# Performance work log

Measured on AMD Instinct MI355X. Metric: run time of the kernel, lower is better.

The kernel has to match this reference:

```python
import jax, jax.numpy as jnp
import numpy as np

B, L, V, H, N, NL = 32, 1024, 32000, 512, 64, 4


def setup_inputs() -> dict:
    key = jax.random.key(0)
    ks = jax.random.split(key, 10)
    x = jax.random.randint(ks[0], (B, L), 0, V)
    embedding = jax.random.normal(ks[1], (V, H), jnp.float32) * 0.02
    # S4D-style init: dt log-uniform in [1e-3, 1e-1], A = -0.5 + i*pi*n (S4D-Lin)
    log_dt = jax.random.uniform(ks[2], (NL, H), jnp.float32,
                                minval=np.log(1e-3), maxval=np.log(1e-1))
    A_log = jnp.log(0.5 * jnp.ones((NL, H, N), jnp.float32))
    A_imag = jnp.broadcast_to(np.pi * jnp.arange(N, dtype=jnp.float32), (NL, H, N))
    C_re = jax.random.normal(ks[3], (NL, H, N), jnp.float32) * (0.5 ** 0.5)
    C_im = jax.random.normal(ks[4], (NL, H, N), jnp.float32) * (0.5 ** 0.5)
    D = jax.random.normal(ks[5], (NL, H), jnp.float32)
    fc_w = jax.random.normal(ks[6], (1, H), jnp.float32) * (1.0 / np.sqrt(H))
    fc_b = jnp.zeros((1,), jnp.float32)
    return {"x": x, "embedding": embedding, "log_dt": log_dt, "A_log": A_log,
            "A_imag": A_imag, "C_re": C_re, "C_im": C_im, "D": D,
            "fc_w": fc_w, "fc_b": fc_b}


def _s4d_layer(u, log_dt, A_log, A_imag, C_re, C_im, D):
    # u: [B, L, H] -> channels-first [B, H, L]
    Lx = u.shape[1]
    ub = jnp.transpose(u, (0, 2, 1))
    dt = jnp.exp(log_dt)                              # [H]
    A = -jnp.exp(A_log) + 1j * A_imag                 # [H, N]
    dtA = dt[:, None] * A                             # [H, N]
    C = C_re + 1j * C_im
    Ct = C * (jnp.exp(dtA) - 1.0) / A                 # ZOH-discretized C*B
    t = jnp.arange(Lx, dtype=jnp.float32)
    vand = jnp.exp(dtA[:, :, None] * t)               # [H, N, L] Vandermonde
    K = 2.0 * jnp.einsum('hn,hnl->hl', Ct, vand).real # [H, L] SSM kernel
    n = 2 * Lx                                        # linear conv via padded FFT
    y = jnp.fft.irfft(jnp.fft.rfft(ub, n=n) * jnp.fft.rfft(K, n=n), n=n)[..., :Lx]
    y = y + D[:, None] * ub                           # skip connection
    y = jax.nn.gelu(y)
    return jnp.transpose(y, (0, 2, 1))                # [B, L, H]


def reference(x, embedding, log_dt, A_log, A_imag, C_re, C_im, D, fc_w, fc_b):
    h = embedding[x]                                  # [B, L, H]
    for i in range(log_dt.shape[0]):                  # small fixed layer count
        h = _s4d_layer(h, log_dt[i], A_log[i], A_imag[i],
                       C_re[i], C_im[i], D[i])
    pooled = h.mean(axis=1)                           # [B, H]
    out = pooled @ fc_w.T + fc_b                      # [B, 1]
    return out.squeeze(1)                             # [B]
```

## Files before the change

### kernel.cpp

```cpp
#include <hip/hip_runtime.h>
#include <math.h>

static const int kB = 32;
static const int kL = 1024;
static const int kH = 512;
static const int kN = 64;
static const int kNL = 4;
static const int kNFFT = 2048;

#define TWO_PI 6.283185307179586476925286766559

typedef float v2f __attribute__((ext_vector_type(2)));

__device__ __forceinline__ v2f cmul(v2f a, v2f b) {
    v2f axx = __builtin_shufflevector(a, a, 0, 0);
    v2f ayy = __builtin_shufflevector(a, a, 1, 1);
    v2f byx = __builtin_shufflevector(b, b, 1, 0);
    v2f t = ayy * byx;
    t.x = -t.x;
    return axx * b + t;
}

template<bool INV>
__device__ __forceinline__ v2f jrot(v2f t) {
    v2f r = __builtin_shufflevector(t, t, 1, 0);
    if (!INV) { r.y = -r.y; } else { r.x = -r.x; }
    return r;
}

#define LDSZ 2176
__device__ __forceinline__ constexpr int swoff(int LGM, int u) {
    return (LGM == 0) ? u : (LGM == 3) ? (8 * u + (u >> 1)) : (68 * u);
}

template<bool INV>
__device__ __forceinline__ void dft8(const v2f c[8], v2f y[8]) {
    const float s = 0.70710678118654752440f;
    v2f t0 = c[0] + c[4], t1 = c[0] - c[4];
    v2f t2 = c[2] + c[6], t3 = c[2] - c[6];
    v2f e0 = t0 + t2, e2 = t0 - t2;
    v2f j3 = jrot<INV>(t3);
    v2f e1 = t1 + j3, e3 = t1 - j3;

    t0 = c[1] + c[5]; t1 = c[1] - c[5];
    t2 = c[3] + c[7]; t3 = c[3] - c[7];
    v2f o0 = t0 + t2, o2 = t0 - t2;
    v2f j3o = jrot<INV>(t3);
    v2f o1 = t1 + j3o, o3 = t1 - j3o;

    if (!INV) {
        v2f r1 = __builtin_shufflevector(o1, o1, 1, 0);
        o1 = s * (v2f){o1.x + r1.x, o1.y - r1.y};
        v2f r2 = __builtin_shufflevector(o2, o2, 1, 0);
        o2 = (v2f){r2.x, -r2.y};
        v2f r3 = __builtin_shufflevector(o3, o3, 1, 0);
        o3 = s * (v2f){r3.x - o3.x, -r3.y - o3.y};
    } else {
        v2f r1 = __builtin_shufflevector(o1, o1, 1, 0);
        o1 = s * (v2f){o1.x - r1.x, o1.y + r1.y};
        v2f r2 = __builtin_shufflevector(o2, o2, 1, 0);
        o2 = (v2f){-r2.x, r2.y};
        v2f r3 = __builtin_shufflevector(o3, o3, 1, 0);
        o3 = s * (v2f){-(o3.x + r3.x), r3.y - o3.y};
    }
    y[0] = e0 + o0; y[4] = e0 - o0;
    y[1] = e1 + o1; y[5] = e1 - o1;
    y[2] = e2 + o2; y[6] = e2 - o2;
    y[3] = e3 + o3; y[7] = e3 - o3;
}

__device__ __forceinline__ void dft8h(const v2f c[4], v2f y[8]) {
    const float s = 0.70710678118654752440f;
    v2f e0 = c[0] + c[2], e2 = c[0] - c[2];
    v2f j  = jrot<false>(c[2]);
    v2f e1 = c[0] + j, e3 = c[0] - j;
    v2f o0 = c[1] + c[3], o2 = c[1] - c[3];
    v2f jo = jrot<false>(c[3]);
    v2f o1 = c[1] + jo, o3 = c[1] - jo;

    v2f r1 = __builtin_shufflevector(o1, o1, 1, 0);
    o1 = s * (v2f){o1.x + r1.x, o1.y - r1.y};
    v2f r2 = __builtin_shufflevector(o2, o2, 1, 0);
    o2 = (v2f){r2.x, -r2.y};
    v2f r3 = __builtin_shufflevector(o3, o3, 1, 0);
    o3 = s * (v2f){r3.x - o3.x, -r3.y - o3.y};

    y[0] = e0 + o0; y[4] = e0 - o0;
    y[1] = e1 + o1; y[5] = e1 - o1;
    y[2] = e2 + o2; y[6] = e2 - o2;
    y[3] = e3 + o3; y[7] = e3 - o3;
}

template<bool INV, int LGM>
__device__ __forceinline__ void stage8_write(v2f* lds, int tid, v2f y[8]) {
    const int m = 1 << LGM;
    const int jm = tid & ~(m - 1);
    float rev = (INV ? (1.0f / 2048.0f) : (-1.0f / 2048.0f)) * (float)jm;
    v2f w1 = { __builtin_amdgcn_cosf(rev), __builtin_amdgcn_sinf(rev) };
    v2f w2 = cmul(w1, w1);
    v2f w3 = cmul(w2, w1);
    v2f w4 = cmul(w2, w2);
    v2f w5 = cmul(w3, w2);
    v2f w6 = cmul(w3, w3);
    v2f w7 = cmul(w4, w3);
    int base = ((tid >> LGM) << (LGM + 3)) + (tid & (m - 1));
    int swb = base + (base >> 4);
    lds[swb + swoff(LGM, 0)] = y[0];
    lds[swb + swoff(LGM, 1)] = cmul(w1, y[1]);
    lds[swb + swoff(LGM, 2)] = cmul(w2, y[2]);
    lds[swb + swoff(LGM, 3)] = cmul(w3, y[3]);
    lds[swb + swoff(LGM, 4)] = cmul(w4, y[4]);
    lds[swb + swoff(LGM, 5)] = cmul(w5, y[5]);
    lds[swb + swoff(LGM, 6)] = cmul(w6, y[6]);
    lds[swb + swoff(LGM, 7)] = cmul(w7, y[7]);
}

__device__ __forceinline__ void read8(const v2f* lds, int swb, v2f c[8]) {
#pragma unroll
    for (int s = 0; s < 8; ++s) c[s] = lds[swb + 272 * s];
}

__device__ __forceinline__ v2f gelu2(v2f v) {
    v2f v2 = v * v;
    v2f q = v2 * 0.044715f + 1.0f;
    v2f z = v * q * 1.5957691216057308f;
    v2f e;
    e.x = __expf(z.x); e.y = __expf(z.y);
    v2f den = e + 1.0f;
    v2f r;
    r.x = __builtin_amdgcn_rcpf(den.x);
    r.y = __builtin_amdgcn_rcpf(den.y);
    return v - v * r;
}

__global__ __launch_bounds__(256) void embed_kernel(const int* __restrict__ x,
                                                    const float* __restrict__ emb,
                                                    float* __restrict__ act)
{
    __shared__ float tile[64][65];
    int hb = blockIdx.x, lb = blockIdx.y, b = blockIdx.z;
    int h0 = hb * 64, l0 = lb * 64;
    int tid = threadIdx.x;
#pragma unroll
    for (int k = 0; k < 16; ++k) {
        int idx = (k << 8) + tid;
        int li = idx >> 6, hi = idx & 63;
        int xv = x[b * kL + l0 + li];
        tile[li][hi] = emb[(size_t)xv * kH + h0 + hi];
    }
    __syncthreads();
#pragma unroll
    for (int k = 0; k < 16; ++k) {
        int idx = (k << 8) + tid;
        int hi = idx >> 6, li = idx & 63;
        act[((size_t)b * kH + h0 + hi) * kL + l0 + li] = tile[li][hi];
    }
}

__global__ __launch_bounds__(256) void kcomp_kernel(const float* __restrict__ log_dt,
                                                    const float* __restrict__ A_log,
                                                    const float* __restrict__ A_imag,
                                                    const float* __restrict__ C_re,
                                                    const float* __restrict__ C_im,
                                                    v2f* __restrict__ Khat,
                                                    int layer0, int out_stride)
{
    __shared__ v2f lds[LDSZ];
    __shared__ float dre_s[kN], g2re_s[kN], g2im_s[kN], hi_s[kN], lo_s[kN];
    __shared__ v2f w256_s[kN];

    int h = blockIdx.x, tid = threadIdx.x;
    int layer = layer0 + blockIdx.y;
    int swbase = tid + (tid >> 4);
    const size_t po = (size_t)layer * kH + h;

    if (tid < kN) {
        int n = tid;
        float dt  = expf(log_dt[po]);
        float Are = -expf(A_log[po * kN + n]);
        float Aim = A_imag[po * kN + n];
        float dre = dt * Are;
        float dim = dt * Aim;
        float er = expf(dre);
        float sw, cw;
        sincosf(dim, &sw, &cw);
        float emr = er * cw - 1.0f, emi = er * sw;
        float inv = 1.0f / (Are * Are + Aim * Aim);
        float air = Are * inv, aii = -Aim * inv;
        float br = emr * air - emi * aii;
        float bi = emr * aii + emi * air;
        float cr = C_re[po * kN + n], ci = C_im[po * kN + n];
        dre_s[n]  = dre;
        g2re_s[n] = 2.0f * (cr * br - ci * bi);
        g2im_s[n] = 2.0f * (cr * bi + ci * br);
        double dimrev = (double)dim * (1.0 / TWO_PI);
        float drf = (float)dimrev;
        float hi = __uint_as_float(__float_as_uint(drf) & 0xFFFFF000u);
        hi_s[n] = hi;
        lo_s[n] = (float)(dimrev - (double)hi);
        float mag256 = __expf(dre * 256.0f);
        double r2 = dimrev * 256.0;
        r2 -= floor(r2);
        float fr2 = (float)r2;
        w256_s[n] = (v2f){mag256 * __builtin_amdgcn_cosf(fr2),
                          mag256 * __builtin_amdgcn_sinf(fr2)};
    }
    __syncthreads();

    float acc0 = 0.f, acc1 = 0.f, acc2 = 0.f, acc3 = 0.f;
    const float lf = (float)tid;
    for (int n = 0; n < kN; ++n) {
        float dre  = dre_s[n];
        float g2re = g2re_s[n], g2im = g2im_s[n];
        float t1 = hi_s[n] * lf;
        float r1 = t1 - floorf(t1);
        float rv = r1 + lo_s[n] * lf;
        rv -= floorf(rv);
        float mag = __expf(dre * lf);
        float sp = __builtin_amdgcn_sinf(rv);
        float cp = __builtin_amdgcn_cosf(rv);
        float pzx = mag * cp, pzy = mag * sp;
        v2f w = w256_s[n];
        float tx;
        acc0 += g2re * pzx - g2im * pzy;
        tx = pzx * w.x - pzy * w.y; pzy = pzx * w.y + pzy * w.x; pzx = tx;
        acc1 += g2re * pzx - g2im * pzy;
        tx = pzx * w.x - pzy * w.y; pzy = pzx * w.y + pzy * w.x; pzx = tx;
        acc2 += g2re * pzx - g2im * pzy;
        tx = pzx * w.x - pzy * w.y; pzy = pzx * w.y + pzy * w.x; pzx = tx;
        acc3 += g2re * pzx - g2im * pzy;
    }

    {
        v2f c[4], y[8];
        c[0] = (v2f){acc0, 0.f}; c[1] = (v2f){acc1, 0.f};
        c[2] = (v2f){acc2, 0.f}; c[3] = (v2f){acc3, 0.f};
        dft8h(c, y);
        stage8_write<false, 0>(lds, tid, y);
    }
    __syncthreads();
    {
        v2f c[8], y[8];
        read8(lds, swbase, c);
        __syncthreads();
        dft8<false>(c, y);
        stage8_write<false, 3>(lds, tid, y);
    }
    __syncthreads();
    {
        v2f c[8], y[8];
        read8(lds, swbase, c);
        __syncthreads();
        dft8<false>(c, y);
        stage8_write<false, 6>(lds, tid, y);
    }
    __syncthreads();
    {
        const float invn = 1.0f / (float)kNFFT;
        v2f* outp = Khat + (size_t)(layer * out_stride + h) * kNFFT;
#pragma unroll
        for (int r = 0; r < 2; ++r) {
            v2f c0 = lds[swbase + 272 * r];
            v2f c1 = lds[swbase + 272 * r + 544];
            v2f c2 = lds[swbase + 272 * r + 1088];
            v2f c3 = lds[swbase + 272 * r + 1632];
            v2f t0 = c0 + c2, t1 = c0 - c2;
            v2f t2 = c1 + c3, t3 = c1 - c3;
            v2f j3 = jrot<false>(t3);
            int q = tid + (r << 8);
            outp[q]        = (t0 + t2) * invn;
            outp[q + 512]  = (t1 + j3) * invn;
            outp[q + 1024] = (t0 - t2) * invn;
            outp[q + 1536] = (t1 - j3) * invn;
        }
    }
}

__global__ __launch_bounds__(256) void conv_mega(const float* __restrict__ act,
                                                 const v2f* __restrict__ Khat,
                                                 const float* __restrict__ Dvec,
                                                 const float* __restrict__ fc_w,
                                                 const float* __restrict__ fc_b,
                                                 float* __restrict__ out)
{
    __shared__ v2f lds[LDSZ];
    __shared__ v2f wred[4];

    int h = blockIdx.x, pair = blockIdx.y, tid = threadIdx.x;
    int swbase = tid + (tid >> 4);
    const float* rowa = act + ((size_t)(2 * pair) * kH + h) * kL;
    const float* rowb = rowa + (size_t)kH * kL;

    v2f us[4];
#pragma unroll
    for (int s = 0; s < 4; ++s) {
        int l = tid + (s << 8);
        us[s] = (v2f){rowa[l], rowb[l]};
    }

#pragma unroll 1
    for (int layer = 0; layer < kNL; ++layer) {
        const v2f* kh = Khat + ((size_t)layer * kH + h) * kNFFT;
        float Dh = Dvec[layer * kH + h];

        {
            v2f y[8];
            dft8h(us, y);
            stage8_write<false, 0>(lds, tid, y);
        }
        __syncthreads();
        {
            v2f c[8], y[8];
            read8(lds, swbase, c);
            __syncthreads();
            dft8<false>(c, y);
            stage8_write<false, 3>(lds, tid, y);
        }
        __syncthreads();
        {
            v2f c[8], y[8];
            read8(lds, swbase, c);
            __syncthreads();
            dft8<false>(c, y);
            stage8_write<false, 6>(lds, tid, y);
        }
        __syncthreads();
        {
            v2f cc[2][4];
#pragma unroll
            for (int r = 0; r < 2; ++r)
#pragma unroll
                for (int s = 0; s < 4; ++s)
                    cc[r][s] = lds[swbase + 272 * r + 544 * s];
            __syncthreads();
#pragma unroll
            for (int r = 0; r < 2; ++r) {
                v2f t0 = cc[r][0] + cc[r][2], t1 = cc[r][0] - cc[r][2];
                v2f t2 = cc[r][1] + cc[r][3], t3 = cc[r][1] - cc[r][3];
                v2f j3 = jrot<false>(t3);
                int q = tid + (r << 8);
                int swq = swbase + 272 * r;
                lds[swq]        = cmul(t0 + t2, kh[q]);
                lds[swq + 544]  = cmul(t1 + j3, kh[q + 512]);
                lds[swq + 1088] = cmul(t0 - t2, kh[q + 1024]);
                lds[swq + 1632] = cmul(t1 - j3, kh[q + 1536]);
            }
        }
        __syncthreads();
        {
            v2f c[8], y[8];
            read8(lds, swbase, c);
            __syncthreads();
            dft8<true>(c, y);
            stage8_write<true, 0>(lds, tid, y);
        }
        __syncthreads();
        {
            v2f c[8], y[8];
            read8(lds, swbase, c);
            __syncthreads();
            dft8<true>(c, y);
            stage8_write<true, 3>(lds, tid, y);
        }
        __syncthreads();
        {
            v2f c[8], y[8];
            read8(lds, swbase, c);
            __syncthreads();
            dft8<true>(c, y);
            stage8_write<true, 6>(lds, tid, y);
        }
        __syncthreads();
        {
            v2f cc[2][4];
#pragma unroll
            for (int r = 0; r < 2; ++r)
#pragma unroll
                for (int s = 0; s < 4; ++s)
                    cc[r][s] = lds[swbase + 272 * r + 544 * s];
#pragma unroll
            for (int r = 0; r < 2; ++r) {
                v2f t0 = cc[r][0] + cc[r][2], t1 = cc[r][0] - cc[r][2];
                v2f t2 = cc[r][1] + cc[r][3], t3 = cc[r][1] - cc[r][3];
                v2f j3 = jrot<false>(t3);
                v2f y0 = t0 + t2;
                v2f y1 = t1 - j3;
                us[r]     = gelu2(y0 + Dh * us[r]);
                us[r + 2] = gelu2(y1 + Dh * us[r + 2]);
            }
        }
        __syncthreads();
    }

    v2f p = us[0] + us[1] + us[2] + us[3];
#pragma unroll
    for (int off = 32; off > 0; off >>= 1) {
        p.x += __shfl_down(p.x, off);
        p.y += __shfl_down(p.y, off);
    }
    if ((tid & 63) == 0) wred[tid >> 6] = p;
    __syncthreads();
    if (tid == 0) {
        v2f t = wred[0] + wred[1] + wred[2] + wred[3];
        float scale = fc_w[h] * (1.0f / (float)kL);
        float bias = (h == 0) ? fc_b[0] : 0.0f;
        atomicAdd(out + 2 * pair,     t.x * scale + bias);
        atomicAdd(out + 2 * pair + 1, t.y * scale + bias);
    }
}

__global__ __launch_bounds__(256) void conv_kernel(float* __restrict__ act,
                                                   const v2f* __restrict__ Khat,
                                                   const float* __restrict__ Dvec)
{
    __shared__ v2f lds[LDSZ];

    int h = blockIdx.x, pair = blockIdx.y, tid = threadIdx.x;
    int swbase = tid + (tid >> 4);
    float* rowa = act + ((size_t)(2 * pair) * kH + h) * kL;
    float* rowb = rowa + (size_t)kH * kL;

    v2f us[4];
#pragma unroll
    for (int s = 0; s < 4; ++s) {
        int l = tid + (s << 8);
        us[s] = (v2f){rowa[l], rowb[l]};
    }
    {
        v2f y[8];
        dft8h(us, y);
        stage8_write<false, 0>(lds, tid, y);
    }
    __syncthreads();
    {
        v2f c[8], y[8];
        read8(lds, swbase, c);
        __syncthreads();
        dft8<false>(c, y);
        stage8_write<false, 3>(lds, tid, y);
    }
    __syncthreads();
    {
        v2f c[8], y[8];
        read8(lds, swbase, c);
        __syncthreads();
        dft8<false>(c, y);
        stage8_write<false, 6>(lds, tid, y);
    }
    __syncthreads();
    {
        v2f cc[2][4];
#pragma unroll
        for (int r = 0; r < 2; ++r)
#pragma unroll
            for (int s = 0; s < 4; ++s)
                cc[r][s] = lds[swbase + 272 * r + 544 * s];
        __syncthreads();
        const v2f* kh = Khat + (size_t)h * kNFFT;
#pragma unroll
        for (int r = 0; r < 2; ++r) {
            v2f t0 = cc[r][0] + cc[r][2], t1 = cc[r][0] - cc[r][2];
            v2f t2 = cc[r][1] + cc[r][3], t3 = cc[r][1] - cc[r][3];
            v2f j3 = jrot<false>(t3);
            int q = tid + (r << 8);
            int swq = swbase + 272 * r;
            lds[swq]        = cmul(t0 + t2, kh[q]);
            lds[swq + 544]  = cmul(t1 + j3, kh[q + 512]);
            lds[swq + 1088] = cmul(t0 - t2, kh[q + 1024]);
            lds[swq + 1632] = cmul(t1 - j3, kh[q + 1536]);
        }
    }
    __syncthreads();
    {
        v2f c[8], y[8];
        read8(lds, swbase, c);
        __syncthreads();
        dft8<true>(c, y);
        stage8_write<true, 0>(lds, tid, y);
    }
    __syncthreads();
    {
        v2f c[8], y[8];
        read8(lds, swbase, c);
        __syncthreads();
        dft8<true>(c, y);
        stage8_write<true, 3>(lds, tid, y);
    }
    __syncthreads();
    {
        v2f c[8], y[8];
        read8(lds, swbase, c);
        __syncthreads();
        dft8<true>(c, y);
        stage8_write<true, 6>(lds, tid, y);
    }
    __syncthreads();
    {
        float Dh = Dvec[h];
#pragma unroll
        for (int r = 0; r < 2; ++r) {
            v2f c0 = lds[swbase + 272 * r];
            v2f c1 = lds[swbase + 272 * r + 544];
            v2f c2 = lds[swbase + 272 * r + 1088];
            v2f c3 = lds[swbase + 272 * r + 1632];
            v2f t0 = c0 + c2, t1 = c0 - c2;
            v2f t2 = c1 + c3, t3 = c1 - c3;
            v2f j3 = jrot<false>(t3);
            v2f y0 = t0 + t2;
            v2f y1 = t1 - j3;
            int l0 = tid + (r << 8);
            v2f g0 = gelu2(y0 + Dh * us[r]);
            v2f g1 = gelu2(y1 + Dh * us[r + 2]);
            rowa[l0]       = g0.x;
            rowb[l0]       = g0.y;
            rowa[l0 + 512] = g1.x;
            rowb[l0 + 512] = g1.y;
        }
    }
}

__global__ __launch_bounds__(256) void final_kernel(const float* __restrict__ act,
                                                    const float* __restrict__ fc_w,
                                                    const float* __restrict__ fc_b,
                                                    float* __restrict__ out)
{
    int hb = blockIdx.x, b = blockIdx.y, tid = threadIdx.x;
    float acc = 0.f;
    for (int hh = 0; hh < 32; ++hh) {
        int h = hb * 32 + hh;
        float w = fc_w[h];
        const float* row = act + ((size_t)b * kH + h) * kL;
#pragma unroll
        for (int l = tid; l < kL; l += 256) acc += row[l] * w;
    }
    __shared__ float red[256];
    red[tid] = acc;
    __syncthreads();
    for (int s = 128; s > 0; s >>= 1) {
        if (tid < s) red[tid] += red[tid + s];
        __syncthreads();
    }
    if (tid == 0) {
        float v = red[0] * (1.0f / (float)kL);
        if (hb == 0) v += fc_b[0];
        atomicAdd(out + b, v);
    }
}

extern "C" void kernel_launch(void* const* d_in, const int* in_sizes, int n_in,
                              void* d_out, int out_size, void* d_ws, size_t ws_size,
                              hipStream_t stream)
{
    const int*   x         = (const int*)d_in[0];
    const float* embedding = (const float*)d_in[1];
    const float* log_dt    = (const float*)d_in[2];
    const float* A_log     = (const float*)d_in[3];
    const float* A_imag    = (const float*)d_in[4];
    const float* C_re      = (const float*)d_in[5];
    const float* C_im      = (const float*)d_in[6];
    const float* Dv        = (const float*)d_in[7];
    const float* fc_w      = (const float*)d_in[8];
    const float* fc_b      = (const float*)d_in[9];
    float* out = (float*)d_out;

    char* ws = (char*)d_ws;
    const size_t act_bytes  = (size_t)kB * kH * kL * sizeof(float);
    const size_t khat_bytes = (size_t)kH * kNFFT * sizeof(float) * 2;
    float* act = (float*)ws;
    v2f*   Khat = (v2f*)(ws + act_bytes);

    const bool multi = ws_size >= act_bytes + kNL * khat_bytes;

    hipMemsetAsync(d_out, 0, (size_t)out_size * sizeof(float), stream);
    embed_kernel<<<dim3(8, 16, 32), 256, 0, stream>>>(x, embedding, act);

    if (multi) {
        kcomp_kernel<<<dim3(kH, kNL), 256, 0, stream>>>(log_dt, A_log, A_imag,
                                                        C_re, C_im, Khat, 0, kH);
        conv_mega<<<dim3(kH, kB / 2), 256, 0, stream>>>(act, Khat, Dv,
                                                        fc_w, fc_b, out);
    } else {
        for (int layer = 0; layer < kNL; ++layer) {
            kcomp_kernel<<<dim3(kH, 1), 256, 0, stream>>>(log_dt, A_log, A_imag,
                                                          C_re, C_im, Khat, layer, 0);
            conv_kernel<<<dim3(kH, kB / 2), 256, 0, stream>>>(act, Khat, Dv + layer * kH);
        }
        final_kernel<<<dim3(16, kB), 256, 0, stream>>>(act, fc_w, fc_b, out);
    }
}
```

Before: 334.6 us.

## Keep activations in LDS, raise occupancy bound, drop redundant barrier, reorder grid

Moves the per-thread activation state of the fused multi-layer conv kernel from registers into a shared-memory array and adds a minimum-blocks-per-CU launch bound of 6. Together these are meant to cut register pressure and allow more resident blocks. It also removes the barrier between the reads and writes of the radix-4/kernel-multiply stage, which is safe because each thread rewrites only the addresses it read. Finally it swaps the grid dimensions so that blocks sharing the same H-channel Khat are scheduled adjacently for cache reuse. The costs are extra LDS traffic and a larger shared-memory footprint per block, plus possible spills if the register cap is too tight.

```diff
diff --git a/kernel.cpp b/kernel.cpp
--- a/kernel.cpp
+++ b/kernel.cpp
@@ -276,26 +276,26 @@
     }
 }
 
-__global__ __launch_bounds__(256) void conv_mega(const float* __restrict__ act,
-                                                 const v2f* __restrict__ Khat,
-                                                 const float* __restrict__ Dvec,
-                                                 const float* __restrict__ fc_w,
-                                                 const float* __restrict__ fc_b,
-                                                 float* __restrict__ out)
+__global__ __launch_bounds__(256, 6) void conv_mega(const float* __restrict__ act,
+                                                    const v2f* __restrict__ Khat,
+                                                    const float* __restrict__ Dvec,
+                                                    const float* __restrict__ fc_w,
+                                                    const float* __restrict__ fc_b,
+                                                    float* __restrict__ out)
 {
     __shared__ v2f lds[LDSZ];
+    __shared__ v2f us_lds[4][256];
     __shared__ v2f wred[4];
 
-    int h = blockIdx.x, pair = blockIdx.y, tid = threadIdx.x;
+    int pair = blockIdx.x, h = blockIdx.y, tid = threadIdx.x;
     int swbase = tid + (tid >> 4);
     const float* rowa = act + ((size_t)(2 * pair) * kH + h) * kL;
     const float* rowb = rowa + (size_t)kH * kL;
 
-    v2f us[4];
 #pragma unroll
     for (int s = 0; s < 4; ++s) {
         int l = tid + (s << 8);
-        us[s] = (v2f){rowa[l], rowb[l]};
+        us_lds[s][tid] = (v2f){rowa[l], rowb[l]};
     }
 
 #pragma unroll 1
@@ -304,8 +304,10 @@
         float Dh = Dvec[layer * kH + h];
 
         {
-            v2f y[8];
-            dft8h(us, y);
+            v2f c[4], y[8];
+#pragma unroll
+            for (int s = 0; s < 4; ++s) c[s] = us_lds[s][tid];
+            dft8h(c, y);
             stage8_write<false, 0>(lds, tid, y);
         }
         __syncthreads();
@@ -326,20 +328,17 @@
         }
         __syncthreads();
         {
-            v2f cc[2][4];
-#pragma unroll
-            for (int r = 0; r < 2; ++r)
-#pragma unroll
-                for (int s = 0; s < 4; ++s)
-                    cc[r][s] = lds[swbase + 272 * r + 544 * s];
-            __syncthreads();
 #pragma unroll
             for (int r = 0; r < 2; ++r) {
-                v2f t0 = cc[r][0] + cc[r][2], t1 = cc[r][0] - cc[r][2];
-                v2f t2 = cc[r][1] + cc[r][3], t3 = cc[r][1] - cc[r][3];
+                int swq = swbase + 272 * r;
+                v2f c0 = lds[swq];
+                v2f c1 = lds[swq + 544];
+                v2f c2 = lds[swq + 1088];
+                v2f c3 = lds[swq + 1632];
+                v2f t0 = c0 + c2, t1 = c0 - c2;
+                v2f t2 = c1 + c3, t3 = c1 - c3;
                 v2f j3 = jrot<false>(t3);
                 int q = tid + (r << 8);
-                int swq = swbase + 272 * r;
                 lds[swq]        = cmul(t0 + t2, kh[q]);
                 lds[swq + 544]  = cmul(t1 + j3, kh[q + 512]);
                 lds[swq + 1088] = cmul(t0 - t2, kh[q + 1024]);
@@ -372,27 +371,26 @@
         }
         __syncthreads();
         {
-            v2f cc[2][4];
-#pragma unroll
-            for (int r = 0; r < 2; ++r)
-#pragma unroll
-                for (int s = 0; s < 4; ++s)
-                    cc[r][s] = lds[swbase + 272 * r + 544 * s];
 #pragma unroll
             for (int r = 0; r < 2; ++r) {
-                v2f t0 = cc[r][0] + cc[r][2], t1 = cc[r][0] - cc[r][2];
-                v2f t2 = cc[r][1] + cc[r][3], t3 = cc[r][1] - cc[r][3];
+                int swq = swbase + 272 * r;
+                v2f c0 = lds[swq];
+                v2f c1 = lds[swq + 544];
+                v2f c2 = lds[swq + 1088];
+                v2f c3 = lds[swq + 1632];
+                v2f t0 = c0 + c2, t1 = c0 - c2;
+                v2f t2 = c1 + c3, t3 = c1 - c3;
                 v2f j3 = jrot<false>(t3);
                 v2f y0 = t0 + t2;
                 v2f y1 = t1 - j3;
-                us[r]     = gelu2(y0 + Dh * us[r]);
-                us[r + 2] = gelu2(y1 + Dh * us[r + 2]);
+                us_lds[r][tid]     = gelu2(y0 + Dh * us_lds[r][tid]);
+                us_lds[r + 2][tid] = gelu2(y1 + Dh * us_lds[r + 2][tid]);
             }
         }
         __syncthreads();
     }
 
-    v2f p = us[0] + us[1] + us[2] + us[3];
+    v2f p = us_lds[0][tid] + us_lds[1][tid] + us_lds[2][tid] + us_lds[3][tid];
 #pragma unroll
     for (int off = 32; off > 0; off >>= 1) {
         p.x += __shfl_down(p.x, off);
@@ -449,21 +447,18 @@
     }
     __syncthreads();
     {
-        v2f cc[2][4];
-#pragma unroll
-        for (int r = 0; r < 2; ++r)
-#pragma unroll
-            for (int s = 0; s < 4; ++s)
-                cc[r][s] = lds[swbase + 272 * r + 544 * s];
-        __syncthreads();
         const v2f* kh = Khat + (size_t)h * kNFFT;
 #pragma unroll
         for (int r = 0; r < 2; ++r) {
-            v2f t0 = cc[r][0] + cc[r][2], t1 = cc[r][0] - cc[r][2];
-            v2f t2 = cc[r][1] + cc[r][3], t3 = cc[r][1] - cc[r][3];
+            int swq = swbase + 272 * r;
+            v2f c0 = lds[swq];
+            v2f c1 = lds[swq + 544];
+            v2f c2 = lds[swq + 1088];
+            v2f c3 = lds[swq + 1632];
+            v2f t0 = c0 + c2, t1 = c0 - c2;
+            v2f t2 = c1 + c3, t3 = c1 - c3;
             v2f j3 = jrot<false>(t3);
             int q = tid + (r << 8);
-            int swq = swbase + 272 * r;
             lds[swq]        = cmul(t0 + t2, kh[q]);
             lds[swq + 544]  = cmul(t1 + j3, kh[q + 512]);
             lds[swq + 1088] = cmul(t0 - t2, kh[q + 1024]);
@@ -577,7 +572,7 @@
     if (multi) {
         kcomp_kernel<<<dim3(kH, kNL), 256, 0, stream>>>(log_dt, A_log, A_imag,
                                                         C_re, C_im, Khat, 0, kH);
-        conv_mega<<<dim3(kH, kB / 2), 256, 0, stream>>>(act, Khat, Dv,
+        conv_mega<<<dim3(kB / 2, kH), 256, 0, stream>>>(act, Khat, Dv,
                                                         fc_w, fc_b, out);
     } else {
         for (int layer = 0; layer < kNL; ++layer) {
```

After: 908.0 us. +171.3%, slower.

## Split fused multi-layer conv into per-layer kernels and use precomputed twiddle table

Applied to the files above, without the earlier changes.

Replaces the single kernel that ran all four S4D layers per channel with three per-layer conv kernels plus a final conv kernel that fuses pooling and the output projection. Adds a small kernel that precomputes FFT twiddle factors into a global table, so FFT stages load twiddles instead of computing sin/cos and the power chain. A conjugate-multiply variant handles the inverse FFT. The unfused layers now write and reread the full activation tensor in global memory between layers, which adds substantial memory traffic in exchange for possibly lower register pressure per kernel.

```diff
diff --git a/kernel.cpp b/kernel.cpp
--- a/kernel.cpp
+++ b/kernel.cpp
@@ -19,6 +19,15 @@
     v2f t = ayy * byx;
     t.x = -t.x;
     return axx * b + t;
+}
+
+__device__ __forceinline__ v2f cmulc(v2f a, v2f b) {
+    v2f axx = __builtin_shufflevector(a, a, 0, 0);
+    v2f ayy = __builtin_shufflevector(a, a, 1, 1);
+    v2f byx = __builtin_shufflevector(b, b, 1, 0);
+    v2f t = axx * b;
+    t.y = -t.y;
+    return ayy * byx + t;
 }
 
 template<bool INV>
@@ -92,27 +101,33 @@
 }
 
 template<bool INV, int LGM>
-__device__ __forceinline__ void stage8_write(v2f* lds, int tid, v2f y[8]) {
+__device__ __forceinline__ void stage8_write(v2f* lds, int tid, v2f y[8],
+                                             const v2f* __restrict__ tw) {
     const int m = 1 << LGM;
-    const int jm = tid & ~(m - 1);
-    float rev = (INV ? (1.0f / 2048.0f) : (-1.0f / 2048.0f)) * (float)jm;
-    v2f w1 = { __builtin_amdgcn_cosf(rev), __builtin_amdgcn_sinf(rev) };
-    v2f w2 = cmul(w1, w1);
-    v2f w3 = cmul(w2, w1);
-    v2f w4 = cmul(w2, w2);
-    v2f w5 = cmul(w3, w2);
-    v2f w6 = cmul(w3, w3);
-    v2f w7 = cmul(w4, w3);
+    const int tsel = (LGM == 0) ? 0 : (LGM == 3) ? 1 : 2;
+    const v2f* twp = tw + (tsel * 256 + tid) * 7;
+    v2f w1 = twp[0], w2 = twp[1], w3 = twp[2], w4 = twp[3];
+    v2f w5 = twp[4], w6 = twp[5], w7 = twp[6];
     int base = ((tid >> LGM) << (LGM + 3)) + (tid & (m - 1));
     int swb = base + (base >> 4);
     lds[swb + swoff(LGM, 0)] = y[0];
-    lds[swb + swoff(LGM, 1)] = cmul(w1, y[1]);
-    lds[swb + swoff(LGM, 2)] = cmul(w2, y[2]);
-    lds[swb + swoff(LGM, 3)] = cmul(w3, y[3]);
-    lds[swb + swoff(LGM, 4)] = cmul(w4, y[4]);
-    lds[swb + swoff(LGM, 5)] = cmul(w5, y[5]);
-    lds[swb + swoff(LGM, 6)] = cmul(w6, y[6]);
-    lds[swb + swoff(LGM, 7)] = cmul(w7, y[7]);
+    if (!INV) {
+        lds[swb + swoff(LGM, 1)] = cmul(w1, y[1]);
+        lds[swb + swoff(LGM, 2)] = cmul(w2, y[2]);
+        lds[swb + swoff(LGM, 3)] = cmul(w3, y[3]);
+        lds[swb + swoff(LGM, 4)] = cmul(w4, y[4]);
+        lds[swb + swoff(LGM, 5)] = cmul(w5, y[5]);
+        lds[swb + swoff(LGM, 6)] = cmul(w6, y[6]);
+        lds[swb + swoff(LGM, 7)] = cmul(w7, y[7]);
+    } else {
+        lds[swb + swoff(LGM, 1)] = cmulc(y[1], w1);
+        lds[swb + swoff(LGM, 2)] = cmulc(y[2], w2);
+        lds[swb + swoff(LGM, 3)] = cmulc(y[3], w3);
+        lds[swb + swoff(LGM, 4)] = cmulc(y[4], w4);
+        lds[swb + swoff(LGM, 5)] = cmulc(y[5], w5);
+        lds[swb + swoff(LGM, 6)] = cmulc(y[6], w6);
+        lds[swb + swoff(LGM, 7)] = cmulc(y[7], w7);
+    }
 }
 
 __device__ __forceinline__ void read8(const v2f* lds, int swb, v2f c[8]) {
@@ -133,6 +148,21 @@
     return v - v * r;
 }
 
+__global__ __launch_bounds__(256) void twfill_kernel(v2f* __restrict__ tw)
+{
+    int tid = threadIdx.x;
+    const int lgms[3] = {0, 3, 6};
+#pragma unroll
+    for (int t = 0; t < 3; ++t) {
+        int m = 1 << lgms[t];
+        int jm = tid & ~(m - 1);
+        for (int u = 1; u <= 7; ++u) {
+            double ang = -TWO_PI * (double)(jm * u) / 2048.0;
+            tw[(t * 256 + tid) * 7 + (u - 1)] = (v2f){(float)cos(ang), (float)sin(ang)};
+        }
+    }
+}
+
 __global__ __launch_bounds__(256) void embed_kernel(const int* __restrict__ x,
                                                     const float* __restrict__ emb,
                                                     float* __restrict__ act)
@@ -163,6 +193,7 @@
                                                     const float* __restrict__ C_re,
                                                     const float* __restrict__ C_im,
                                                     v2f* __restrict__ Khat,
+                                                    const v2f* __restrict__ tw,
                                                     int layer0, int out_stride)
 {
     __shared__ v2f lds[LDSZ];
@@ -236,7 +267,7 @@
         c[0] = (v2f){acc0, 0.f}; c[1] = (v2f){acc1, 0.f};
         c[2] = (v2f){acc2, 0.f}; c[3] = (v2f){acc3, 0.f};
         dft8h(c, y);
-        stage8_write<false, 0>(lds, tid, y);
+        stage8_write<false, 0>(lds, tid, y, tw);
     }
     __syncthreads();
     {
@@ -244,7 +275,7 @@
         read8(lds, swbase, c);
         __syncthreads();
         dft8<false>(c, y);
-        stage8_write<false, 3>(lds, tid, y);
+        stage8_write<false, 3>(lds, tid, y, tw);
     }
     __syncthreads();
     {
@@ -252,7 +283,7 @@
         read8(lds, swbase, c);
         __syncthreads();
         dft8<false>(c, y);
-        stage8_write<false, 6>(lds, tid, y);
+        stage8_write<false, 6>(lds, tid, y, tw);
     }
     __syncthreads();
     {
@@ -276,141 +307,9 @@
     }
 }
 
-__global__ __launch_bounds__(256) void conv_mega(const float* __restrict__ act,
-                                                 const v2f* __restrict__ Khat,
-                                                 const float* __restrict__ Dvec,
-                                                 const float* __restrict__ fc_w,
-                                                 const float* __restrict__ fc_b,
-                                                 float* __restrict__ out)
-{
-    __shared__ v2f lds[LDSZ];
-    __shared__ v2f wred[4];
-
-    int h = blockIdx.x, pair = blockIdx.y, tid = threadIdx.x;
-    int swbase = tid + (tid >> 4);
-    const float* rowa = act + ((size_t)(2 * pair) * kH + h) * kL;
-    const float* rowb = rowa + (size_t)kH * kL;
-
-    v2f us[4];
-#pragma unroll
-    for (int s = 0; s < 4; ++s) {
-        int l = tid + (s << 8);
-        us[s] = (v2f){rowa[l], rowb[l]};
-    }
-
-#pragma unroll 1
-    for (int layer = 0; layer < kNL; ++layer) {
-        const v2f* kh = Khat + ((size_t)layer * kH + h) * kNFFT;
-        float Dh = Dvec[layer * kH + h];
-
-        {
-            v2f y[8];
-            dft8h(us, y);
-            stage8_write<false, 0>(lds, tid, y);
-        }
-        __syncthreads();
-        {
-            v2f c[8], y[8];
-            read8(lds, swbase, c);
-            __syncthreads();
-            dft8<false>(c, y);
-            stage8_write<false, 3>(lds, tid, y);
-        }
-        __syncthreads();
-        {
-            v2f c[8], y[8];
-            read8(lds, swbase, c);
-            __syncthreads();
-            dft8<false>(c, y);
-            stage8_write<false, 6>(lds, tid, y);
-        }
-        __syncthreads();
-        {
-            v2f cc[2][4];
-#pragma unroll
-            for (int r = 0; r < 2; ++r)
-#pragma unroll
-                for (int s = 0; s < 4; ++s)
-                    cc[r][s] = lds[swbase + 272 * r + 544 * s];
-            __syncthreads();
-#pragma unroll
-            for (int r = 0; r < 2; ++r) {
-                v2f t0 = cc[r][0] + cc[r][2], t1 = cc[r][0] - cc[r][2];
-                v2f t2 = cc[r][1] + cc[r][3], t3 = cc[r][1] - cc[r][3];
-                v2f j3 = jrot<false>(t3);
-                int q = tid + (r << 8);
-                int swq = swbase + 272 * r;
-                lds[swq]        = cmul(t0 + t2, kh[q]);
-                lds[swq + 544]  = cmul(t1 + j3, kh[q + 512]);
-                lds[swq + 1088] = cmul(t0 - t2, kh[q + 1024]);
-                lds[swq + 1632] = cmul(t1 - j3, kh[q + 1536]);
-            }
-        }
-        __syncthreads();
-        {
-            v2f c[8], y[8];
-            read8(lds, swbase, c);
-            __syncthreads();
-            dft8<true>(c, y);
-            stage8_write<true, 0>(lds, tid, y);
-        }
-        __syncthreads();
-        {
-            v2f c[8], y[8];
-            read8(lds, swbase, c);
-            __syncthreads();
-            dft8<true>(c, y);
-            stage8_write<true, 3>(lds, tid, y);
-        }
-        __syncthreads();
-        {
-            v2f c[8], y[8];
-            read8(lds, swbase, c);
-            __syncthreads();
-            dft8<true>(c, y);
-            stage8_write<true, 6>(lds, tid, y);
-        }
-        __syncthreads();
-        {
-            v2f cc[2][4];
-#pragma unroll
-            for (int r = 0; r < 2; ++r)
-#pragma unroll
-                for (int s = 0; s < 4; ++s)
-                    cc[r][s] = lds[swbase + 272 * r + 544 * s];
-#pragma unroll
-            for (int r = 0; r < 2; ++r) {
-                v2f t0 = cc[r][0] + cc[r][2], t1 = cc[r][0] - cc[r][2];
-                v2f t2 = cc[r][1] + cc[r][3], t3 = cc[r][1] - cc[r][3];
-                v2f j3 = jrot<false>(t3);
-                v2f y0 = t0 + t2;
-                v2f y1 = t1 - j3;
-                us[r]     = gelu2(y0 + Dh * us[r]);
-                us[r + 2] = gelu2(y1 + Dh * us[r + 2]);
-            }
-        }
-        __syncthreads();
-    }
-
-    v2f p = us[0] + us[1] + us[2] + us[3];
-#pragma unroll
-    for (int off = 32; off > 0; off >>= 1) {
-        p.x += __shfl_down(p.x, off);
-        p.y += __shfl_down(p.y, off);
-    }
-    if ((tid & 63) == 0) wred[tid >> 6] = p;
-    __syncthreads();
-    if (tid == 0) {
-        v2f t = wred[0] + wred[1] + wred[2] + wred[3];
-        float scale = fc_w[h] * (1.0f / (float)kL);
-        float bias = (h == 0) ? fc_b[0] : 0.0f;
-        atomicAdd(out + 2 * pair,     t.x * scale + bias);
-        atomicAdd(out + 2 * pair + 1, t.y * scale + bias);
-    }
-}
-
 __global__ __launch_bounds__(256) void conv_kernel(float* __restrict__ act,
                                                    const v2f* __restrict__ Khat,
+                                                   const v2f* __restrict__ tw,
                                                    const float* __restrict__ Dvec)
 {
     __shared__ v2f lds[LDSZ];
@@ -429,7 +328,7 @@
     {
         v2f y[8];
         dft8h(us, y);
-        stage8_write<false, 0>(lds, tid, y);
+        stage8_write<false, 0>(lds, tid, y, tw);
     }
     __syncthreads();
     {
@@ -437,7 +336,7 @@
         read8(lds, swbase, c);
         __syncthreads();
         dft8<false>(c, y);
-        stage8_write<false, 3>(lds, tid, y);
+        stage8_write<false, 3>(lds, tid, y, tw);
     }
     __syncthreads();
     {
@@ -445,7 +344,7 @@
         read8(lds, swbase, c);
         __syncthreads();
         dft8<false>(c, y);
-        stage8_write<false, 6>(lds, tid, y);
+        stage8_write<false, 6>(lds, tid, y, tw);
     }
     __syncthreads();
     {
@@ -476,7 +375,7 @@
         read8(lds, swbase, c);
         __syncthreads();
         dft8<true>(c, y);
-        stage8_write<true, 0>(lds, tid, y);
+        stage8_write<true, 0>(lds, tid, y, tw);
     }
     __syncthreads();
     {
@@ -484,7 +383,7 @@
         read8(lds, swbase, c);
         __syncthreads();
         dft8<true>(c, y);
-        stage8_write<true, 3>(lds, tid, y);
+        stage8_write<true, 3>(lds, tid, y, tw);
     }
     __syncthreads();
     {
@@ -492,7 +391,7 @@
         read8(lds, swbase, c);
         __syncthreads();
         dft8<true>(c, y);
-        stage8_write<true, 6>(lds, tid, y);
+        stage8_write<true, 6>(lds, tid, y, tw);
     }
     __syncthreads();
     {
@@ -519,31 +418,128 @@
     }
 }
 
-__global__ __launch_bounds__(256) void final_kernel(const float* __restrict__ act,
-                                                    const float* __restrict__ fc_w,
-                                                    const float* __restrict__ fc_b,
-                                                    float* __restrict__ out)
+__global__ __launch_bounds__(256) void conv_final(const float* __restrict__ act,
+                                                  const v2f* __restrict__ Khat,
+                                                  const v2f* __restrict__ tw,
+                                                  const float* __restrict__ Dvec,
+                                                  const float* __restrict__ fc_w,
+                                                  const float* __restrict__ fc_b,
+                                                  float* __restrict__ out)
 {
-    int hb = blockIdx.x, b = blockIdx.y, tid = threadIdx.x;
-    float acc = 0.f;
-    for (int hh = 0; hh < 32; ++hh) {
-        int h = hb * 32 + hh;
-        float w = fc_w[h];
-        const float* row = act + ((size_t)b * kH + h) * kL;
-#pragma unroll
-        for (int l = tid; l < kL; l += 256) acc += row[l] * w;
-    }
-    __shared__ float red[256];
-    red[tid] = acc;
-    __syncthreads();
-    for (int s = 128; s > 0; s >>= 1) {
-        if (tid < s) red[tid] += red[tid + s];
-        __syncthreads();
-    }
+    __shared__ v2f lds[LDSZ];
+    __shared__ v2f wred[4];
+
+    int h = blockIdx.x, pair = blockIdx.y, tid = threadIdx.x;
+    int swbase = tid + (tid >> 4);
+    const float* rowa = act + ((size_t)(2 * pair) * kH + h) * kL;
+    const float* rowb = rowa + (size_t)kH * kL;
+
+    v2f us[4];
+#pragma unroll
+    for (int s = 0; s < 4; ++s) {
+        int l = tid + (s << 8);
+        us[s] = (v2f){rowa[l], rowb[l]};
+    }
+    {
+        v2f y[8];
+        dft8h(us, y);
+        stage8_write<false, 0>(lds, tid, y, tw);
+    }
+    __syncthreads();
+    {
+        v2f c[8], y[8];
+        read8(lds, swbase, c);
+        __syncthreads();
+        dft8<false>(c, y);
+        stage8_write<false, 3>(lds, tid, y, tw);
+    }
+    __syncthreads();
+    {
+        v2f c[8], y[8];
+        read8(lds, swbase, c);
+        __syncthreads();
+        dft8<false>(c, y);
+        stage8_write<false, 6>(lds, tid, y, tw);
+    }
+    __syncthreads();
+    {
+        v2f cc[2][4];
+#pragma unroll
+        for (int r = 0; r < 2; ++r)
+#pragma unroll
+            for (int s = 0; s < 4; ++s)
+                cc[r][s] = lds[swbase + 272 * r + 544 * s];
+        __syncthreads();
+        const v2f* kh = Khat + (size_t)h * kNFFT;
+#pragma unroll
+        for (int r = 0; r < 2; ++r) {
+            v2f t0 = cc[r][0] + cc[r][2], t1 = cc[r][0] - cc[r][2];
+            v2f t2 = cc[r][1] + cc[r][3], t3 = cc[r][1] - cc[r][3];
+            v2f j3 = jrot<false>(t3);
+            int q = tid + (r << 8);
+            int swq = swbase + 272 * r;
+            lds[swq]        = cmul(t0 + t2, kh[q]);
+            lds[swq + 544]  = cmul(t1 + j3, kh[q + 512]);
+            lds[swq + 1088] = cmul(t0 - t2, kh[q + 1024]);
+            lds[swq + 1632] = cmul(t1 - j3, kh[q + 1536]);
+        }
+    }
+    __syncthreads();
+    {
+        v2f c[8], y[8];
+        read8(lds, swbase, c);
+        __syncthreads();
+        dft8<true>(c, y);
+        stage8_write<true, 0>(lds, tid, y, tw);
+    }
+    __syncthreads();
+    {
+        v2f c[8], y[8];
+        read8(lds, swbase, c);
+        __syncthreads();
+        dft8<true>(c, y);
+        stage8_write<true, 3>(lds, tid, y, tw);
+    }
+    __syncthreads();
+    {
+        v2f c[8], y[8];
+        read8(lds, swbase, c);
+        __syncthreads();
+        dft8<true>(c, y);
+        stage8_write<true, 6>(lds, tid, y, tw);
+    }
+    __syncthreads();
+    v2f p = (v2f){0.f, 0.f};
+    {
+        float Dh = Dvec[h];
+#pragma unroll
+        for (int r = 0; r < 2; ++r) {
+            v2f c0 = lds[swbase + 272 * r];
+            v2f c1 = lds[swbase + 272 * r + 544];
+            v2f c2 = lds[swbase + 272 * r + 1088];
+            v2f c3 = lds[swbase + 272 * r + 1632];
+            v2f t0 = c0 + c2, t1 = c0 - c2;
+            v2f t2 = c1 + c3, t3 = c1 - c3;
+            v2f j3 = jrot<false>(t3);
+            v2f y0 = t0 + t2;
+            v2f y1 = t1 - j3;
+            p += gelu2(y0 + Dh * us[r]);
+            p += gelu2(y1 + Dh * us[r + 2]);
+        }
+    }
+#pragma unroll
+    for (int off = 32; off > 0; off >>= 1) {
+        p.x += __shfl_down(p.x, off);
+        p.y += __shfl_down(p.y, off);
+    }
+    if ((tid & 63) == 0) wred[tid >> 6] = p;
+    __syncthreads();
     if (tid == 0) {
-        float v = red[0] * (1.0f / (float)kL);
-        if (hb == 0) v += fc_b[0];
-        atomicAdd(out + b, v);
+        v2f t = wred[0] + wred[1] + wred[2] + wred[3];
+        float scale = fc_w[h] * (1.0f / (float)kL);
+        float bias = (h == 0) ? fc_b[0] : 0.0f;
+        atomicAdd(out + 2 * pair,     t.x * scale + bias);
+        atomicAdd(out + 2 * pair + 1, t.y * scale + bias);
     }
 }
 
@@ -564,27 +560,38 @@
     float* out = (float*)d_out;
 
     char* ws = (char*)d_ws;
+    const size_t tw_bytes   = 64 * 1024;
     const size_t act_bytes  = (size_t)kB * kH * kL * sizeof(float);
     const size_t khat_bytes = (size_t)kH * kNFFT * sizeof(float) * 2;
-    float* act = (float*)ws;
-    v2f*   Khat = (v2f*)(ws + act_bytes);
-
-    const bool multi = ws_size >= act_bytes + kNL * khat_bytes;
+    v2f*   tw   = (v2f*)ws;
+    float* act  = (float*)(ws + tw_bytes);
+    v2f*   Khat = (v2f*)(ws + tw_bytes + act_bytes);
+
+    const bool multi = ws_size >= tw_bytes + act_bytes + kNL * khat_bytes;
 
     hipMemsetAsync(d_out, 0, (size_t)out_size * sizeof(float), stream);
+    twfill_kernel<<<1, 256, 0, stream>>>(tw);
     embed_kernel<<<dim3(8, 16, 32), 256, 0, stream>>>(x, embedding, act);
 
     if (multi) {
         kcomp_kernel<<<dim3(kH, kNL), 256, 0, stream>>>(log_dt, A_log, A_imag,
-                                                        C_re, C_im, Khat, 0, kH);
-        conv_mega<<<dim3(kH, kB / 2), 256, 0, stream>>>(act, Khat, Dv,
-                                                        fc_w, fc_b, out);
+                                                        C_re, C_im, Khat, tw, 0, kH);
+        for (int layer = 0; layer < kNL - 1; ++layer) {
+            conv_kernel<<<dim3(kH, kB / 2), 256, 0, stream>>>(
+                act, Khat + (size_t)layer * kH * kNFFT, tw, Dv + layer * kH);
+        }
+        conv_final<<<dim3(kH, kB / 2), 256, 0, stream>>>(
+            act, Khat + (size_t)(kNL - 1) * kH * kNFFT, tw,
+            Dv + (kNL - 1) * kH, fc_w, fc_b, out);
     } else {
-        for (int layer = 0; layer < kNL; ++layer) {
+        for (int layer = 0; layer < kNL - 1; ++layer) {
             kcomp_kernel<<<dim3(kH, 1), 256, 0, stream>>>(log_dt, A_log, A_imag,
-                                                          C_re, C_im, Khat, layer, 0);
-            conv_kernel<<<dim3(kH, kB / 2), 256, 0, stream>>>(act, Khat, Dv + layer * kH);
-        }
-        final_kernel<<<dim3(16, kB), 256, 0, stream>>>(act, fc_w, fc_b, out);
-    }
-}
+                                                          C_re, C_im, Khat, tw, layer, 0);
+            conv_kernel<<<dim3(kH, kB / 2), 256, 0, stream>>>(act, Khat, tw, Dv + layer * kH);
+        }
+        kcomp_kernel<<<dim3(kH, 1), 256, 0, stream>>>(log_dt, A_log, A_imag,
+                                                      C_re, C_im, Khat, tw, kNL - 1, 0);
+        conv_final<<<dim3(kH, kB / 2), 256, 0, stream>>>(act, Khat, tw,
+                                                         Dv + (kNL - 1) * kH, fc_w, fc_b, out);
+    }
+}
```

After: 455.7 us. +36.2%, slower.

## Split fused multi-layer conv into per-layer kernels with deterministic final reduction

Applied to the files above, without the earlier changes.

Replaces the single kernel that ran all four S4D layers with activations held in registers. It now launches one conv kernel per layer that round-trips activations through global memory, then a last-layer kernel that writes per-channel pooled partials into a workspace buffer. A small reduce kernel sums those partials and adds the bias, replacing the memset and atomicAdd accumulation. This makes the output deterministic and cuts per-block register and loop overhead, at the cost of several extra full reads and writes of the activation tensor and more kernel launches.

```diff
diff --git a/kernel.cpp b/kernel.cpp
--- a/kernel.cpp
+++ b/kernel.cpp
@@ -276,139 +276,6 @@
     }
 }
 
-__global__ __launch_bounds__(256) void conv_mega(const float* __restrict__ act,
-                                                 const v2f* __restrict__ Khat,
-                                                 const float* __restrict__ Dvec,
-                                                 const float* __restrict__ fc_w,
-                                                 const float* __restrict__ fc_b,
-                                                 float* __restrict__ out)
-{
-    __shared__ v2f lds[LDSZ];
-    __shared__ v2f wred[4];
-
-    int h = blockIdx.x, pair = blockIdx.y, tid = threadIdx.x;
-    int swbase = tid + (tid >> 4);
-    const float* rowa = act + ((size_t)(2 * pair) * kH + h) * kL;
-    const float* rowb = rowa + (size_t)kH * kL;
-
-    v2f us[4];
-#pragma unroll
-    for (int s = 0; s < 4; ++s) {
-        int l = tid + (s << 8);
-        us[s] = (v2f){rowa[l], rowb[l]};
-    }
-
-#pragma unroll 1
-    for (int layer = 0; layer < kNL; ++layer) {
-        const v2f* kh = Khat + ((size_t)layer * kH + h) * kNFFT;
-        float Dh = Dvec[layer * kH + h];
-
-        {
-            v2f y[8];
-            dft8h(us, y);
-            stage8_write<false, 0>(lds, tid, y);
-        }
-        __syncthreads();
-        {
-            v2f c[8], y[8];
-            read8(lds, swbase, c);
-            __syncthreads();
-            dft8<false>(c, y);
-            stage8_write<false, 3>(lds, tid, y);
-        }
-        __syncthreads();
-        {
-            v2f c[8], y[8];
-            read8(lds, swbase, c);
-            __syncthreads();
-            dft8<false>(c, y);
-            stage8_write<false, 6>(lds, tid, y);
-        }
-        __syncthreads();
-        {
-            v2f cc[2][4];
-#pragma unroll
-            for (int r = 0; r < 2; ++r)
-#pragma unroll
-                for (int s = 0; s < 4; ++s)
-                    cc[r][s] = lds[swbase + 272 * r + 544 * s];
-            __syncthreads();
-#pragma unroll
-            for (int r = 0; r < 2; ++r) {
-                v2f t0 = cc[r][0] + cc[r][2], t1 = cc[r][0] - cc[r][2];
-                v2f t2 = cc[r][1] + cc[r][3], t3 = cc[r][1] - cc[r][3];
-                v2f j3 = jrot<false>(t3);
-                int q = tid + (r << 8);
-                int swq = swbase + 272 * r;
-                lds[swq]        = cmul(t0 + t2, kh[q]);
-                lds[swq + 544]  = cmul(t1 + j3, kh[q + 512]);
-                lds[swq + 1088] = cmul(t0 - t2, kh[q + 1024]);
-                lds[swq + 1632] = cmul(t1 - j3, kh[q + 1536]);
-            }
-        }
-        __syncthreads();
-        {
-            v2f c[8], y[8];
-            read8(lds, swbase, c);
-            __syncthreads();
-            dft8<true>(c, y);
-            stage8_write<true, 0>(lds, tid, y);
-        }
-        __syncthreads();
-        {
-            v2f c[8], y[8];
-            read8(lds, swbase, c);
-            __syncthreads();
-            dft8<true>(c, y);
-            stage8_write<true, 3>(lds, tid, y);
-        }
-        __syncthreads();
-        {
-            v2f c[8], y[8];
-            read8(lds, swbase, c);
-            __syncthreads();
-            dft8<true>(c, y);
-            stage8_write<true, 6>(lds, tid, y);
-        }
-        __syncthreads();
-        {
-            v2f cc[2][4];
-#pragma unroll
-            for (int r = 0; r < 2; ++r)
-#pragma unroll
-                for (int s = 0; s < 4; ++s)
-                    cc[r][s] = lds[swbase + 272 * r + 544 * s];
-#pragma unroll
-            for (int r = 0; r < 2; ++r) {
-                v2f t0 = cc[r][0] + cc[r][2], t1 = cc[r][0] - cc[r][2];
-                v2f t2 = cc[r][1] + cc[r][3], t3 = cc[r][1] - cc[r][3];
-                v2f j3 = jrot<false>(t3);
-                v2f y0 = t0 + t2;
-                v2f y1 = t1 - j3;
-                us[r]     = gelu2(y0 + Dh * us[r]);
-                us[r + 2] = gelu2(y1 + Dh * us[r + 2]);
-            }
-        }
-        __syncthreads();
-    }
-
-    v2f p = us[0] + us[1] + us[2] + us[3];
-#pragma unroll
-    for (int off = 32; off > 0; off >>= 1) {
-        p.x += __shfl_down(p.x, off);
-        p.y += __shfl_down(p.y, off);
-    }
-    if ((tid & 63) == 0) wred[tid >> 6] = p;
-    __syncthreads();
-    if (tid == 0) {
-        v2f t = wred[0] + wred[1] + wred[2] + wred[3];
-        float scale = fc_w[h] * (1.0f / (float)kL);
-        float bias = (h == 0) ? fc_b[0] : 0.0f;
-        atomicAdd(out + 2 * pair,     t.x * scale + bias);
-        atomicAdd(out + 2 * pair + 1, t.y * scale + bias);
-    }
-}
-
 __global__ __launch_bounds__(256) void conv_kernel(float* __restrict__ act,
                                                    const v2f* __restrict__ Khat,
                                                    const float* __restrict__ Dvec)
@@ -519,31 +386,146 @@
     }
 }
 
-__global__ __launch_bounds__(256) void final_kernel(const float* __restrict__ act,
-                                                    const float* __restrict__ fc_w,
-                                                    const float* __restrict__ fc_b,
-                                                    float* __restrict__ out)
+__global__ __launch_bounds__(256) void conv_final(const float* __restrict__ act,
+                                                  const v2f* __restrict__ Khat,
+                                                  const float* __restrict__ Dvec,
+                                                  const float* __restrict__ fc_w,
+                                                  v2f* __restrict__ partials)
 {
-    int hb = blockIdx.x, b = blockIdx.y, tid = threadIdx.x;
-    float acc = 0.f;
-    for (int hh = 0; hh < 32; ++hh) {
-        int h = hb * 32 + hh;
-        float w = fc_w[h];
-        const float* row = act + ((size_t)b * kH + h) * kL;
-#pragma unroll
-        for (int l = tid; l < kL; l += 256) acc += row[l] * w;
-    }
-    __shared__ float red[256];
-    red[tid] = acc;
-    __syncthreads();
-    for (int s = 128; s > 0; s >>= 1) {
-        if (tid < s) red[tid] += red[tid + s];
-        __syncthreads();
-    }
+    __shared__ v2f lds[LDSZ];
+    __shared__ v2f wred[4];
+
+    int h = blockIdx.x, pair = blockIdx.y, tid = threadIdx.x;
+    int swbase = tid + (tid >> 4);
+    const float* rowa = act + ((size_t)(2 * pair) * kH + h) * kL;
+    const float* rowb = rowa + (size_t)kH * kL;
+
+    v2f us[4];
+#pragma unroll
+    for (int s = 0; s < 4; ++s) {
+        int l = tid + (s << 8);
+        us[s] = (v2f){rowa[l], rowb[l]};
+    }
+    {
+        v2f y[8];
+        dft8h(us, y);
+        stage8_write<false, 0>(lds, tid, y);
+    }
+    __syncthreads();
+    {
+        v2f c[8], y[8];
+        read8(lds, swbase, c);
+        __syncthreads();
+        dft8<false>(c, y);
+        stage8_write<false, 3>(lds, tid, y);
+    }
+    __syncthreads();
+    {
+        v2f c[8], y[8];
+        read8(lds, swbase, c);
+        __syncthreads();
+        dft8<false>(c, y);
+        stage8_write<false, 6>(lds, tid, y);
+    }
+    __syncthreads();
+    {
+        v2f cc[2][4];
+#pragma unroll
+        for (int r = 0; r < 2; ++r)
+#pragma unroll
+            for (int s = 0; s < 4; ++s)
+                cc[r][s] = lds[swbase + 272 * r + 544 * s];
+        __syncthreads();
+        const v2f* kh = Khat + (size_t)h * kNFFT;
+#pragma unroll
+        for (int r = 0; r < 2; ++r) {
+            v2f t0 = cc[r][0] + cc[r][2], t1 = cc[r][0] - cc[r][2];
+            v2f t2 = cc[r][1] + cc[r][3], t3 = cc[r][1] - cc[r][3];
+            v2f j3 = jrot<false>(t3);
+            int q = tid + (r << 8);
+            int swq = swbase + 272 * r;
+            lds[swq]        = cmul(t0 + t2, kh[q]);
+            lds[swq + 544]  = cmul(t1 + j3, kh[q + 512]);
+            lds[swq + 1088] = cmul(t0 - t2, kh[q + 1024]);
+            lds[swq + 1632] = cmul(t1 - j3, kh[q + 1536]);
+        }
+    }
+    __syncthreads();
+    {
+        v2f c[8], y[8];
+        read8(lds, swbase, c);
+        __syncthreads();
+        dft8<true>(c, y);
+        stage8_write<true, 0>(lds, tid, y);
+    }
+    __syncthreads();
+    {
+        v2f c[8], y[8];
+        read8(lds, swbase, c);
+        __syncthreads();
+        dft8<true>(c, y);
+        stage8_write<true, 3>(lds, tid, y);
+    }
+    __syncthreads();
+    {
+        v2f c[8], y[8];
+        read8(lds, swbase, c);
+        __syncthreads();
+        dft8<true>(c, y);
+        stage8_write<true, 6>(lds, tid, y);
+    }
+    __syncthreads();
+    v2f p = (v2f){0.f, 0.f};
+    {
+        float Dh = Dvec[h];
+#pragma unroll
+        for (int r = 0; r < 2; ++r) {
+            v2f c0 = lds[swbase + 272 * r];
+            v2f c1 = lds[swbase + 272 * r + 544];
+            v2f c2 = lds[swbase + 272 * r + 1088];
+            v2f c3 = lds[swbase + 272 * r + 1632];
+            v2f t0 = c0 + c2, t1 = c0 - c2;
+            v2f t2 = c1 + c3, t3 = c1 - c3;
+            v2f j3 = jrot<false>(t3);
+            v2f y0 = t0 + t2;
+            v2f y1 = t1 - j3;
+            p += gelu2(y0 + Dh * us[r]);
+            p += gelu2(y1 + Dh * us[r + 2]);
+        }
+    }
+#pragma unroll
+    for (int off = 32; off > 0; off >>= 1) {
+        p.x += __shfl_down(p.x, off);
+        p.y += __shfl_down(p.y, off);
+    }
+    if ((tid & 63) == 0) wred[tid >> 6] = p;
+    __syncthreads();
     if (tid == 0) {
-        float v = red[0] * (1.0f / (float)kL);
-        if (hb == 0) v += fc_b[0];
-        atomicAdd(out + b, v);
+        v2f t = wred[0] + wred[1] + wred[2] + wred[3];
+        float scale = fc_w[h] * (1.0f / (float)kL);
+        partials[(size_t)pair * kH + h] = t * scale;
+    }
+}
+
+__global__ __launch_bounds__(256) void reduce_kernel(const v2f* __restrict__ partials,
+                                                     const float* __restrict__ fc_b,
+                                                     float* __restrict__ out)
+{
+    __shared__ v2f wred[4];
+    int pair = blockIdx.x, tid = threadIdx.x;
+    v2f p = partials[(size_t)pair * kH + tid] + partials[(size_t)pair * kH + tid + 256];
+#pragma unroll
+    for (int off = 32; off > 0; off >>= 1) {
+        p.x += __shfl_down(p.x, off);
+        p.y += __shfl_down(p.y, off);
+    }
+    if ((tid & 63) == 0) wred[tid >> 6] = p;
+    __syncthreads();
+    if (tid == 0) {
+        v2f t = wred[0] + wred[1] + wred[2] + wred[3];
+        float bias = fc_b[0];
+        out[2 * pair]     = t.x + bias;
+        out[2 * pair + 1] = t.y + bias;
     }
 }
 
@@ -566,25 +548,36 @@
     char* ws = (char*)d_ws;
     const size_t act_bytes  = (size_t)kB * kH * kL * sizeof(float);
     const size_t khat_bytes = (size_t)kH * kNFFT * sizeof(float) * 2;
-    float* act = (float*)ws;
+    float* act  = (float*)ws;
     v2f*   Khat = (v2f*)(ws + act_bytes);
 
     const bool multi = ws_size >= act_bytes + kNL * khat_bytes;
 
-    hipMemsetAsync(d_out, 0, (size_t)out_size * sizeof(float), stream);
     embed_kernel<<<dim3(8, 16, 32), 256, 0, stream>>>(x, embedding, act);
 
     if (multi) {
+        v2f* partials = Khat;
         kcomp_kernel<<<dim3(kH, kNL), 256, 0, stream>>>(log_dt, A_log, A_imag,
                                                         C_re, C_im, Khat, 0, kH);
-        conv_mega<<<dim3(kH, kB / 2), 256, 0, stream>>>(act, Khat, Dv,
-                                                        fc_w, fc_b, out);
+        for (int layer = 0; layer < kNL - 1; ++layer) {
+            conv_kernel<<<dim3(kH, kB / 2), 256, 0, stream>>>(
+                act, Khat + (size_t)layer * kH * kNFFT, Dv + layer * kH);
+        }
+        conv_final<<<dim3(kH, kB / 2), 256, 0, stream>>>(
+            act, Khat + (size_t)(kNL - 1) * kH * kNFFT,
+            Dv + (kNL - 1) * kH, fc_w, partials);
+        reduce_kernel<<<dim3(kB / 2), 256, 0, stream>>>(partials, fc_b, out);
     } else {
-        for (int layer = 0; layer < kNL; ++layer) {
+        v2f* partials = (v2f*)(ws + act_bytes + khat_bytes);
+        for (int layer = 0; layer < kNL - 1; ++layer) {
             kcomp_kernel<<<dim3(kH, 1), 256, 0, stream>>>(log_dt, A_log, A_imag,
                                                           C_re, C_im, Khat, layer, 0);
             conv_kernel<<<dim3(kH, kB / 2), 256, 0, stream>>>(act, Khat, Dv + layer * kH);
         }
-        final_kernel<<<dim3(16, kB), 256, 0, stream>>>(act, fc_w, fc_b, out);
-    }
-}
+        kcomp_kernel<<<dim3(kH, 1), 256, 0, stream>>>(log_dt, A_log, A_imag,
+                                                      C_re, C_im, Khat, kNL - 1, 0);
+        conv_final<<<dim3(kH, kB / 2), 256, 0, stream>>>(act, Khat,
+                                                         Dv + (kNL - 1) * kH, fc_w, partials);
+        reduce_kernel<<<dim3(kB / 2), 256, 0, stream>>>(partials, fc_b, out);
+    }
+}
```

Result: faster. 292.8 us (-12.5%).
